# Kernel tuning notes

Hardware: AMD Instinct MI355X
Metric: run time of the kernel (lower is better)

Reference implementation:

```python
import jax, jax.numpy as jnp
import numpy as np

U_FEAT = 100000  # user feature vocab
I_FEAT = 100000  # item feature vocab
D = 64           # embedding dim
N_USERS = 4096   # batch of users
N_ITEMS = 16384  # all items
L_U = 50         # nonzero features per user
L_I = 20         # nonzero features per item


def setup_inputs() -> dict:
    key = jax.random.key(0)
    ks = jax.random.split(key, 9)
    return {
        "user_features_embeddings": jax.random.normal(ks[0], (U_FEAT, D), jnp.float32),
        "item_features_embeddings": jax.random.normal(ks[1], (I_FEAT, D), jnp.float32),
        "user_w": jax.random.normal(ks[2], (U_FEAT,), jnp.float32),
        "item_w": jax.random.normal(ks[3], (I_FEAT,), jnp.float32),
        "global_bias": jax.random.normal(ks[4], (1,), jnp.float32),
        "h1": jax.random.normal(ks[5], (D,), jnp.float32),
        "h2": jax.random.normal(ks[6], (D,), jnp.float32),
        "user_idx": jax.random.randint(ks[7], (N_USERS, L_U), 0, U_FEAT),
        "item_idx": jax.random.randint(ks[8], (N_ITEMS, L_I), 0, I_FEAT),
    }


def _pooled(emb, idx, w, h1):
    # emb: [V, D], idx: [N, L], w: [V]
    g = emb[idx]                                   # [N, L, D] gather
    s = g.sum(axis=1)                              # [N, D] feature-embedding sum
    # FM bi-interaction: 0.5 * (sum^2 - sum of squares)
    bi = 0.5 * (jnp.square(s) - jnp.square(g).sum(axis=1))  # [N, D]
    scalar = bi @ h1 + w[idx].sum(axis=1)          # [N]
    return s, scalar


def reference(user_features_embeddings, item_features_embeddings, user_w, item_w,
              global_bias, h1, h2, user_idx, item_idx):
    su, sc_u = _pooled(user_features_embeddings, user_idx, user_w, h1)
    si, sc_i = _pooled(item_features_embeddings, item_idx, item_w, h1)
    ones_u = jnp.ones((su.shape[0], 1), su.dtype)
    ones_i = jnp.ones((si.shape[0], 1), si.dtype)
    # p_u = [sum_emb, h1.bi + sum(w) + bias, 1]; q_v = [sum_emb, 1, h1.bi + sum(w)]
    P = jnp.concatenate([su, (sc_u + global_bias[0])[:, None], ones_u], axis=1)  # [N_USERS, D+2]
    Q = jnp.concatenate([si, ones_i, sc_i[:, None]], axis=1)                     # [N_ITEMS, D+2]
    return P, Q, h2
```

## Files before the change

### kernel.cpp

```cpp
#include <hip/hip_runtime.h>

#define EMB_D 64

template<int L>
__global__ void fm_pool_kernel(const float* __restrict__ emb,
                               const float* __restrict__ w,
                               const int* __restrict__ idx,
                               const float* __restrict__ h1,
                               const float* __restrict__ gbias,
                               int add_bias,
                               int N,
                               float* __restrict__ out,
                               int scalar_col, int one_col) {
  int gtid = blockIdx.x * blockDim.x + threadIdx.x;
  int row  = gtid >> 6;
  int lane = threadIdx.x & 63;
  if (row >= N) return;

  const int* ridx = idx + (size_t)row * L;

  float s = 0.f, sq = 0.f;
#pragma unroll
  for (int l = 0; l < L; ++l) {
    int id  = ridx[l];
    float e = emb[(size_t)id * EMB_D + lane];
    s  += e;
    sq += e * e;
  }

  float wsum = 0.f;
#pragma unroll
  for (int l = lane; l < L; l += 64) wsum += w[ridx[l]];

  float part = 0.5f * (s * s - sq) * h1[lane] + wsum;
#pragma unroll
  for (int off = 32; off >= 1; off >>= 1)
    part += __shfl_down(part, off, 64);

  float* orow = out + (size_t)row * (EMB_D + 2);
  orow[lane] = s;
  if (lane == 0) {
    orow[scalar_col] = part + (add_bias ? gbias[0] : 0.f);
    orow[one_col]    = 1.0f;
  }
}

__global__ void copy_h2_kernel(const float* __restrict__ h2, float* __restrict__ out) {
  out[threadIdx.x] = h2[threadIdx.x];
}

extern "C" void kernel_launch(void* const* d_in, const int* in_sizes, int n_in,
                              void* d_out, int out_size, void* d_ws, size_t ws_size,
                              hipStream_t stream) {
  const float* uemb = (const float*)d_in[0];
  const float* iemb = (const float*)d_in[1];
  const float* uw   = (const float*)d_in[2];
  const float* iw   = (const float*)d_in[3];
  const float* gb   = (const float*)d_in[4];
  const float* h1   = (const float*)d_in[5];
  const float* h2   = (const float*)d_in[6];
  const int*   uidx = (const int*)d_in[7];
  const int*   iidx = (const int*)d_in[8];

  const int NU = 4096, NI = 16384;
  const int LD = EMB_D + 2;

  float* P  = (float*)d_out;
  float* Q  = P + (size_t)NU * LD;
  float* H2 = Q + (size_t)NI * LD;

  dim3 blk(256);

  fm_pool_kernel<50><<<dim3((NU * 64 + 255) / 256), blk, 0, stream>>>(
      uemb, uw, uidx, h1, gb, 1, NU, P, 64, 65);

  fm_pool_kernel<20><<<dim3((NI * 64 + 255) / 256), blk, 0, stream>>>(
      iemb, iw, iidx, h1, gb, 0, NI, Q, 65, 64);

  copy_h2_kernel<<<1, 64, 0, stream>>>(h2, H2);
}
```

Measured before the change: 30.70 us.

## Fuse user, item and h2 kernels into one launch with float4 gathers

Merges the user pooling, item pooling and h2 copy kernels into a single launch where each wave handles one row. Inside a row, the 64 lanes are split into four 16-lane groups that each gather a different feature row with float4 loads, and the partial sums are combined with xor shuffles. This cuts launch overhead and the number of memory instructions per gathered row. In exchange it adds extra shuffle work and leaves lanes idle in the tail and store phases.

```diff
diff --git a/kernel.cpp b/kernel.cpp
--- a/kernel.cpp
+++ b/kernel.cpp
@@ -1,52 +1,95 @@
 #include <hip/hip_runtime.h>
 
 #define EMB_D 64
+#define NU 4096
+#define NI 16384
+#define LDOUT (EMB_D + 2)
+
+__device__ __forceinline__ float4 ld4(const float* p) {
+  return *reinterpret_cast<const float4*>(p);
+}
 
 template<int L>
-__global__ void fm_pool_kernel(const float* __restrict__ emb,
-                               const float* __restrict__ w,
-                               const int* __restrict__ idx,
-                               const float* __restrict__ h1,
-                               const float* __restrict__ gbias,
-                               int add_bias,
-                               int N,
-                               float* __restrict__ out,
-                               int scalar_col, int one_col) {
-  int gtid = blockIdx.x * blockDim.x + threadIdx.x;
-  int row  = gtid >> 6;
-  int lane = threadIdx.x & 63;
-  if (row >= N) return;
+__device__ __forceinline__ void fm_row(const float* __restrict__ emb,
+                                       const float* __restrict__ w,
+                                       const int* __restrict__ idx, int row,
+                                       const float* __restrict__ h1,
+                                       float bias, float* __restrict__ out,
+                                       int scalar_col, int one_col, int lane) {
+  const int* ridx = idx + (size_t)row * L;
+  const int g = lane >> 4;
+  const int sub = lane & 15;
 
-  const int* ridx = idx + (size_t)row * L;
+  float4 s  = make_float4(0.f, 0.f, 0.f, 0.f);
+  float4 sq = make_float4(0.f, 0.f, 0.f, 0.f);
 
-  float s = 0.f, sq = 0.f;
+  constexpr int LM = L & ~3;
 #pragma unroll
-  for (int l = 0; l < L; ++l) {
-    int id  = ridx[l];
-    float e = emb[(size_t)id * EMB_D + lane];
-    s  += e;
-    sq += e * e;
+  for (int l = 0; l < LM; l += 4) {
+    int id = ridx[l + g];
+    float4 e = ld4(emb + (size_t)id * EMB_D + sub * 4);
+    s.x += e.x; s.y += e.y; s.z += e.z; s.w += e.w;
+    sq.x += e.x * e.x; sq.y += e.y * e.y; sq.z += e.z * e.z; sq.w += e.w * e.w;
+  }
+  if constexpr (LM != L) {
+    if (g < (L - LM)) {
+      int id = ridx[LM + g];
+      float4 e = ld4(emb + (size_t)id * EMB_D + sub * 4);
+      s.x += e.x; s.y += e.y; s.z += e.z; s.w += e.w;
+      sq.x += e.x * e.x; sq.y += e.y * e.y; sq.z += e.z * e.z; sq.w += e.w * e.w;
+    }
   }
 
-  float wsum = 0.f;
 #pragma unroll
-  for (int l = lane; l < L; l += 64) wsum += w[ridx[l]];
+  for (int off = 16; off <= 32; off <<= 1) {
+    s.x += __shfl_xor(s.x, off, 64);  s.y += __shfl_xor(s.y, off, 64);
+    s.z += __shfl_xor(s.z, off, 64);  s.w += __shfl_xor(s.w, off, 64);
+    sq.x += __shfl_xor(sq.x, off, 64); sq.y += __shfl_xor(sq.y, off, 64);
+    sq.z += __shfl_xor(sq.z, off, 64); sq.w += __shfl_xor(sq.w, off, 64);
+  }
 
-  float part = 0.5f * (s * s - sq) * h1[lane] + wsum;
+  float part = 0.f;
+  if (g == 0) {
+    float4 h = ld4(h1 + sub * 4);
+    part = 0.5f * ((s.x * s.x - sq.x) * h.x + (s.y * s.y - sq.y) * h.y +
+                   (s.z * s.z - sq.z) * h.z + (s.w * s.w - sq.w) * h.w);
+  }
+  if (lane < L) part += w[ridx[lane]];
+
 #pragma unroll
-  for (int off = 32; off >= 1; off >>= 1)
-    part += __shfl_down(part, off, 64);
+  for (int off = 32; off >= 1; off >>= 1) part += __shfl_down(part, off, 64);
 
-  float* orow = out + (size_t)row * (EMB_D + 2);
-  orow[lane] = s;
+  float* orow = out + (size_t)row * LDOUT;
+  if (g == 0) {
+    *reinterpret_cast<float2*>(orow + sub * 4)     = make_float2(s.x, s.y);
+    *reinterpret_cast<float2*>(orow + sub * 4 + 2) = make_float2(s.z, s.w);
+  }
   if (lane == 0) {
-    orow[scalar_col] = part + (add_bias ? gbias[0] : 0.f);
+    orow[scalar_col] = part + bias;
     orow[one_col]    = 1.0f;
   }
 }
 
-__global__ void copy_h2_kernel(const float* __restrict__ h2, float* __restrict__ out) {
-  out[threadIdx.x] = h2[threadIdx.x];
+__global__ __launch_bounds__(256) void fm_fused(
+    const float* __restrict__ uemb, const float* __restrict__ iemb,
+    const float* __restrict__ uw, const float* __restrict__ iw,
+    const float* __restrict__ gb, const float* __restrict__ h1,
+    const float* __restrict__ h2, const int* __restrict__ uidx,
+    const int* __restrict__ iidx, float* __restrict__ out) {
+  int wid  = blockIdx.x * 4 + (threadIdx.x >> 6);
+  int lane = threadIdx.x & 63;
+
+  float* P  = out;
+  float* Q  = P + (size_t)NU * LDOUT;
+  float* H2 = Q + (size_t)NI * LDOUT;
+
+  if (wid < NU) {
+    fm_row<50>(uemb, uw, uidx, wid, h1, gb[0], P, 64, 65, lane);
+  } else if (wid < NU + NI) {
+    fm_row<20>(iemb, iw, iidx, wid - NU, h1, 0.f, Q, 65, 64, lane);
+  } else if (wid == NU + NI) {
+    H2[lane] = h2[lane];
+  }
 }
 
 extern "C" void kernel_launch(void* const* d_in, const int* in_sizes, int n_in,
@@ -62,20 +105,9 @@
   const int*   uidx = (const int*)d_in[7];
   const int*   iidx = (const int*)d_in[8];
 
-  const int NU = 4096, NI = 16384;
-  const int LD = EMB_D + 2;
+  int nwaves = NU + NI + 1;
+  int nblocks = (nwaves + 3) / 4;
 
-  float* P  = (float*)d_out;
-  float* Q  = P + (size_t)NU * LD;
-  float* H2 = Q + (size_t)NI * LD;
-
-  dim3 blk(256);
-
-  fm_pool_kernel<50><<<dim3((NU * 64 + 255) / 256), blk, 0, stream>>>(
-      uemb, uw, uidx, h1, gb, 1, NU, P, 64, 65);
-
-  fm_pool_kernel<20><<<dim3((NI * 64 + 255) / 256), blk, 0, stream>>>(
-      iemb, iw, iidx, h1, gb, 0, NI, Q, 65, 64);
-
-  copy_h2_kernel<<<1, 64, 0, stream>>>(h2, H2);
+  fm_fused<<<dim3(nblocks), dim3(256), 0, stream>>>(
+      uemb, iemb, uw, iw, gb, h1, h2, uidx, iidx, (float*)d_out);
 }
```

Result: faster. 27.22 us (-11.3%).
